# Performance work log

Hardware: AMD Instinct MI355X
Metric: run time of the kernel (lower is better)

Reference implementation:

```python
import math
import jax, jax.numpy as jnp
import numpy as np

MIN_AMT, MAX_AMT = 1, 32
C = 3
B, H, W = 128, 224, 224


def build_kernel_table():
    # kernels[i] has size = i + MIN_AMT: vertical center column, each channel sums to 1,
    # zero-padded (centered) to MAX_AMT x MAX_AMT (pad_to_width).
    tbl = np.zeros((MAX_AMT - MIN_AMT + 1, MAX_AMT, MAX_AMT, C), np.float32)
    for i, size in enumerate(range(MIN_AMT, MAX_AMT + 1)):
        pad = MAX_AMT - size
        t = pad // 2
        col = t + size // 2
        tbl[i, t:t + size, col, :] = 1.0 / size
    return jnp.asarray(tbl)


def setup_inputs() -> dict:
    key = jax.random.key(0)
    k1, k2, k3 = jax.random.split(key, 3)
    x = jax.random.uniform(k1, (B, H, W, C), jnp.float32)  # image batch
    amt = jax.random.randint(k2, (B,), MIN_AMT, MAX_AMT, dtype=jnp.int32)  # [min, max)
    angles = jax.random.randint(k3, (B,), 0, 91, dtype=jnp.int32)  # degrees [0, 91)
    return {"x": x, "kernels_table": build_kernel_table(), "amt": amt, "angles": angles}


def _rotate_nearest(img, rad):
    # img: (K, K, C); nearest-neighbor rotation about image center (tf.contrib.image.rotate
    # convention: output (x,y) samples input at [cos -sin; sin cos] @ (x,y) + centering offset).
    K = img.shape[0]
    cos, sin = jnp.cos(rad), jnp.sin(rad)
    coords = jnp.arange(K, dtype=jnp.float32)
    yy, xx = jnp.meshgrid(coords, coords, indexing="ij")
    e = jnp.float32(K - 1)
    x_off = (e - (cos * e - sin * e)) * 0.5
    y_off = (e - (sin * e + cos * e)) * 0.5
    sx = cos * xx - sin * yy + x_off
    sy = sin * xx + cos * yy + y_off
    ix = jnp.round(sx).astype(jnp.int32)
    iy = jnp.round(sy).astype(jnp.int32)
    valid = (ix >= 0) & (ix < K) & (iy >= 0) & (iy < K)
    g = img[jnp.clip(iy, 0, K - 1), jnp.clip(ix, 0, K - 1)]  # (K, K, C)
    return jnp.where(valid[..., None], g, jnp.float32(0.0))


def _depthwise_conv(img, ker):
    # img: (H, W, C); ker: (K, K, C) -> per-channel SAME conv, stride 1.
    out = jax.lax.conv_general_dilated(
        img[None], ker[:, :, None, :], (1, 1), "SAME",
        dimension_numbers=("NHWC", "HWIO", "NHWC"), feature_group_count=C)
    return out[0]


def reference(x, kernels_table, amt, angles):
    ker = kernels_table[amt]                                # (B, K, K, C) per-sample gather
    rad = angles.astype(jnp.float32) * jnp.float32(math.pi / 180.0)
    ker = jax.vmap(_rotate_nearest)(ker, rad)               # per-sample rotation
    out = jax.vmap(_depthwise_conv)(x, ker)                 # per-sample depthwise conv
    return out.reshape(-1, 224, 224, 3)
```

## Files before the change

### kernel.cpp

```cpp
#include <hip/hip_runtime.h>
#include <math.h>

namespace {

constexpr int Himg = 224, Wimg = 224, Cn = 3, Kk = 32;
constexpr int MAXT = 64;
constexpr int WSTRIDE = 512;
constexpr int IMG_F  = Himg * Wimg * Cn;
constexpr int ROW_F  = Wimg * Cn;
constexpr int ROW_B  = ROW_F * 4;

constexpr int TW_F = 224;
constexpr int TH = 32;
constexpr int RH = 16;
constexpr int TILES_X = 3;
constexpr int TILES_Y = 7;
constexpr int TPI = TILES_X * TILES_Y;
constexpr int L_W = 320;
constexpr int L_H = TH + 31;
constexpr int L_SZ = L_W * L_H;

typedef float v4  __attribute__((ext_vector_type(4), aligned(4)));
typedef float v4a __attribute__((ext_vector_type(4), aligned(16)));


__global__ __launch_bounds__(64)
void build_taps(const float* __restrict__ tbl,
                const int* __restrict__ amt,
                const int* __restrict__ ang,
                int* __restrict__ ws)
{
    const int b   = blockIdx.x;
    const int tid = threadIdx.x;

    __shared__ int   s_cnt;
    __shared__ float s_w;
    __shared__ int   s_dky[MAXT], s_dkx[MAXT];

    if (tid == 0) { s_cnt = 0; s_w = 0.0f; }
    __syncthreads();

    const int a = amt[b];
    const float  rad = (float)ang[b] * (float)(M_PI / 180.0);
    const double rd  = (double)rad;
    const float  cth = (float)cos(rd);
    const float  sth = (float)sin(rd);
    const float  e   = 31.0f;
    const float xoff = __fmul_rn(__fsub_rn(e, __fsub_rn(__fmul_rn(cth, e), __fmul_rn(sth, e))), 0.5f);
    const float yoff = __fmul_rn(__fsub_rn(e, __fadd_rn(__fmul_rn(sth, e), __fmul_rn(cth, e))), 0.5f);

    for (int p = tid; p < Kk * Kk; p += 64) {
        const int   ky = p >> 5, kx = p & 31;
        const float xf = (float)kx, yf = (float)ky;
        const float sx = __fadd_rn(__fsub_rn(__fmul_rn(cth, xf), __fmul_rn(sth, yf)), xoff);
        const float sy = __fadd_rn(__fadd_rn(__fmul_rn(sth, xf), __fmul_rn(cth, yf)), yoff);
        const int ix = (int)rintf(sx);
        const int iy = (int)rintf(sy);
        if (ix >= 0 && ix < Kk && iy >= 0 && iy < Kk) {
            const float v = tbl[((a * Kk + iy) * Kk + ix) * Cn];
            if (v != 0.0f) {
                const int idx = atomicAdd(&s_cnt, 1);
                if (idx < MAXT) {
                    s_dky[idx] = ky - 15;
                    s_dkx[idx] = kx - 15;
                    s_w = v;
                }
            }
        }
    }
    __syncthreads();

    const int n = min(s_cnt, MAXT);
    int* wsb = ws + b * WSTRIDE;
    if (tid == 0) { wsb[0] = n; wsb[1] = __float_as_int(s_w); }
    for (int i = tid; i < n; i += 64) {
        wsb[2 + i]   = s_dky[i];
        wsb[66 + i]  = s_dkx[i];
        wsb[130 + i] = s_dky[i] * ROW_B + s_dkx[i] * (int)(Cn * sizeof(float));
    }
}

__global__ __launch_bounds__(512, 2)
void blur_w8(const float* __restrict__ x,
             const int* __restrict__ ws,
             float* __restrict__ out,
             int B)
{
    const int tid = threadIdx.x;
    const int L   = blockIdx.x;

    int b, t;
    if (B == 128) {
        const int xcd = L & 7;
        const int j   = L >> 3;
        const int g   = j / TPI;
        t = j - g * TPI;
        b = g * 8 + xcd;
    } else {
        b = L / TPI;
        t = L - b * TPI;
    }
    const int ty = t / TILES_X;
    const int tx = t - ty * TILES_X;
    const int y0 = ty * TH;
    const int g0 = tx * TW_F - 48;
    const int r0 = y0 - 15;

    __shared__ float lds[L_SZ];
    __shared__ int   shNW[2];
    __shared__ int   s_tof[MAXT + 1];

    const int* wsb = ws + b * WSTRIDE;
    if (tid < 2)    shNW[tid] = wsb[tid];
    if (tid < MAXT) {
        const int dky = wsb[2 + tid];
        const int dkx = wsb[66 + tid];
        s_tof[tid] = (dky * L_W + 3 * dkx) * 4;
    }

    const float* xb = x + (size_t)b * IMG_F;
    for (int u = tid; u < L_H * 80; u += 512) {
        const int lr  = u / 80;
        const int lc4 = (u - lr * 80) * 4;
        const int gr  = r0 + lr;
        const int gc  = g0 + lc4;
        v4 val = {0.0f, 0.0f, 0.0f, 0.0f};
        if ((unsigned)gr < (unsigned)Himg && (unsigned)gc < (unsigned)ROW_F)
            val = *(const v4a*)(xb + (size_t)gr * ROW_F + gc);
        *(v4a*)(&lds[lr * L_W + lc4]) = val;
    }
    __syncthreads();

    const int   n = shNW[0];
    const float w = __int_as_float(shNW[1]);

    const int half = tid >> 8;
    const int col  = tid - (half << 8);

    if (col < TW_F) {
        const char* ldsb  = (const char*)lds;
        const int   abase = ((15 + half * RH) * L_W + 48 + col) * 4;

        float acc[RH];
#pragma unroll
        for (int p = 0; p < RH; ++p) acc[p] = 0.0f;

        int tofn = s_tof[0];
        for (int i = 0; i < n; ++i) {
            const int tof = __builtin_amdgcn_readfirstlane(tofn);
            tofn = s_tof[i + 1];
            const char* ap = ldsb + (abase + tof);
#pragma unroll
            for (int p = 0; p < RH; ++p) {
                acc[p] += *(const float*)(ap + p * (L_W * 4));
            }
        }

        float* ob = out + (size_t)b * IMG_F + (size_t)(y0 + half * RH) * ROW_F + tx * TW_F + col;
#pragma unroll
        for (int p = 0; p < RH; ++p) {
            __builtin_nontemporal_store(acc[p] * w, ob + p * ROW_F);
        }
    }
}

}

extern "C" void kernel_launch(void* const* d_in, const int* in_sizes, int n_in,
                              void* d_out, int out_size, void* d_ws, size_t ws_size,
                              hipStream_t stream) {
    const float* x   = (const float*)d_in[0];
    const float* tbl = (const float*)d_in[1];
    const int*   amt = (const int*)d_in[2];
    const int*   ang = (const int*)d_in[3];
    float*       out = (float*)d_out;
    int*         ws  = (int*)d_ws;

    const int B = in_sizes[2];

    build_taps<<<B, 64, 0, stream>>>(tbl, amt, ang, ws);
    blur_w8<<<B * TPI, 512, 0, stream>>>(x, ws, out, B);
}
```

Before: 185.7 us.

## Slide LDS window down column strips with register-prefetched rows

Each block now covers four 28-row tiles in a vertical strip instead of one 32-row tile. Between tiles it shifts the 31-row halo up in LDS and fills in newly loaded rows, and those rows are prefetched into registers while the current tile is being computed. This removes the repeated halo loads from global memory and overlaps loading with compute. In exchange the grid drops to 768 blocks, register pressure rises from the prefetch buffers, and two extra barriers are added per tile.

Result: no change. 189.3 us (+1.9%).

```diff
diff --git a/kernel.cpp b/kernel.cpp
--- a/kernel.cpp
+++ b/kernel.cpp
@@ -11,14 +11,17 @@
 constexpr int ROW_B  = ROW_F * 4;
 
 constexpr int TW_F = 224;
-constexpr int TH = 32;
-constexpr int RH = 16;
+constexpr int TH   = 28;
 constexpr int TILES_X = 3;
-constexpr int TILES_Y = 7;
-constexpr int TPI = TILES_X * TILES_Y;
-constexpr int L_W = 320;
-constexpr int L_H = TH + 31;
+constexpr int TPB  = 4;
+constexpr int RH   = TH / 2;
+constexpr int L_W  = 320;
+constexpr int L_H  = TH + 31;
 constexpr int L_SZ = L_W * L_H;
+constexpr int SH_ROWS = L_H - TH;
+constexpr int SH_CH   = SH_ROWS * 80;
+constexpr int NEW_CH  = TH * 80;
+constexpr int PRO_CH  = L_H * 80;
 
 typedef float v4  __attribute__((ext_vector_type(4), aligned(4)));
 typedef float v4a __attribute__((ext_vector_type(4), aligned(16)));
@@ -81,30 +84,29 @@
 }
 
 __global__ __launch_bounds__(512, 2)
-void blur_w8(const float* __restrict__ x,
-             const int* __restrict__ ws,
-             float* __restrict__ out,
-             int B)
+void blur_slide(const float* __restrict__ x,
+                const int* __restrict__ ws,
+                float* __restrict__ out,
+                int B)
 {
     const int tid = threadIdx.x;
     const int L   = blockIdx.x;
 
-    int b, t;
+    int b, rem;
     if (B == 128) {
         const int xcd = L & 7;
         const int j   = L >> 3;
-        const int g   = j / TPI;
-        t = j - g * TPI;
-        b = g * 8 + xcd;
+        const int g   = j / 6;
+        rem = j - g * 6;
+        b   = g * 8 + xcd;
     } else {
-        b = L / TPI;
-        t = L - b * TPI;
-    }
-    const int ty = t / TILES_X;
-    const int tx = t - ty * TILES_X;
-    const int y0 = ty * TH;
+        b   = L / 6;
+        rem = L - b * 6;
+    }
+    const int tx    = rem >> 1;
+    const int yhalf = rem & 1;
+    const int tyBeg = yhalf * TPB;
     const int g0 = tx * TW_F - 48;
-    const int r0 = y0 - 15;
 
     __shared__ float lds[L_SZ];
     __shared__ int   shNW[2];
@@ -119,48 +121,107 @@
     }
 
     const float* xb = x + (size_t)b * IMG_F;
-    for (int u = tid; u < L_H * 80; u += 512) {
-        const int lr  = u / 80;
-        const int lc4 = (u - lr * 80) * 4;
-        const int gr  = r0 + lr;
-        const int gc  = g0 + lc4;
-        v4 val = {0.0f, 0.0f, 0.0f, 0.0f};
-        if ((unsigned)gr < (unsigned)Himg && (unsigned)gc < (unsigned)ROW_F)
-            val = *(const v4a*)(xb + (size_t)gr * ROW_F + gc);
-        *(v4a*)(&lds[lr * L_W + lc4]) = val;
+
+    {
+        const int r0 = tyBeg * TH - 15;
+        for (int u = tid; u < PRO_CH; u += 512) {
+            const int lr  = u / 80;
+            const int lc4 = (u - lr * 80) * 4;
+            const int gr  = r0 + lr;
+            const int gc  = g0 + lc4;
+            const bool ok = (unsigned)gr < (unsigned)Himg && (unsigned)gc < (unsigned)ROW_F;
+            const float* sp = ok ? (xb + (size_t)gr * ROW_F + gc) : xb;
+            const v4 tv = *(const v4a*)sp;
+            *(v4a*)(&lds[4 * u]) = ok ? tv : v4{0, 0, 0, 0};
+        }
     }
     __syncthreads();
 
     const int   n = shNW[0];
     const float w = __int_as_float(shNW[1]);
-
-    const int half = tid >> 8;
-    const int col  = tid - (half << 8);
-
-    if (col < TW_F) {
-        const char* ldsb  = (const char*)lds;
-        const int   abase = ((15 + half * RH) * L_W + 48 + col) * 4;
-
-        float acc[RH];
-#pragma unroll
-        for (int p = 0; p < RH; ++p) acc[p] = 0.0f;
-
-        int tofn = s_tof[0];
-        for (int i = 0; i < n; ++i) {
-            const int tof = __builtin_amdgcn_readfirstlane(tofn);
-            tofn = s_tof[i + 1];
-            const char* ap = ldsb + (abase + tof);
-#pragma unroll
-            for (int p = 0; p < RH; ++p) {
-                acc[p] += *(const float*)(ap + p * (L_W * 4));
-            }
-        }
-
-        float* ob = out + (size_t)b * IMG_F + (size_t)(y0 + half * RH) * ROW_F + tx * TW_F + col;
-#pragma unroll
-        for (int p = 0; p < RH; ++p) {
-            __builtin_nontemporal_store(acc[p] * w, ob + p * ROW_F);
-        }
+    const int rhalf = tid >> 8;
+    const int col   = tid - (rhalf << 8);
+
+    for (int t = 0; t < TPB; ++t) {
+        const int y0 = (tyBeg + t) * TH;
+
+        v4 rv0{0,0,0,0}, rv1{0,0,0,0}, rv2{0,0,0,0}, rv3{0,0,0,0}, rv4{0,0,0,0};
+        if (t < TPB - 1) {
+#pragma unroll
+            for (int j = 0; j < 5; ++j) {
+                const int v = tid + 512 * j;
+                if (v < NEW_CH) {
+                    const int rr  = v / 80;
+                    const int cc4 = (v - rr * 80) * 4;
+                    const int gr  = y0 + TH + 16 + rr;
+                    const int gc  = g0 + cc4;
+                    const bool ok = (unsigned)gr < (unsigned)Himg && (unsigned)gc < (unsigned)ROW_F;
+                    const float* sp = ok ? (xb + (size_t)gr * ROW_F + gc) : xb;
+                    v4 tv = *(const v4a*)sp;
+                    tv = ok ? tv : v4{0, 0, 0, 0};
+                    if (j == 0) rv0 = tv; else if (j == 1) rv1 = tv; else if (j == 2) rv2 = tv;
+                    else if (j == 3) rv3 = tv; else rv4 = tv;
+                }
+            }
+        }
+
+        if (col < TW_F) {
+            const char* ldsb  = (const char*)lds;
+            const int   abase = ((15 + rhalf * RH) * L_W + 48 + col) * 4;
+
+            float acc[RH];
+#pragma unroll
+            for (int p = 0; p < RH; ++p) acc[p] = 0.0f;
+
+            int tofn = s_tof[0];
+            for (int i = 0; i < n; ++i) {
+                const int tof = __builtin_amdgcn_readfirstlane(tofn);
+                tofn = s_tof[i + 1];
+                const char* ap = ldsb + (abase + tof);
+#pragma unroll
+                for (int p = 0; p < RH; ++p)
+                    acc[p] += *(const float*)(ap + p * (L_W * 4));
+            }
+
+            float* ob = out + (size_t)b * IMG_F
+                      + (size_t)(y0 + rhalf * RH) * ROW_F + tx * TW_F + col;
+#pragma unroll
+            for (int p = 0; p < RH; ++p)
+                __builtin_nontemporal_store(acc[p] * w, ob + p * ROW_F);
+        }
+        if (t == TPB - 1) break;
+
+        v4 sv0{0,0,0,0}, sv1{0,0,0,0}, sv2{0,0,0,0}, sv3{0,0,0,0}, sv4{0,0,0,0};
+#pragma unroll
+        for (int j = 0; j < 5; ++j) {
+            const int v = tid + 512 * j;
+            if (v < SH_CH) {
+                const v4 tv = *(const v4a*)(&lds[TH * L_W + 4 * v]);
+                if (j == 0) sv0 = tv; else if (j == 1) sv1 = tv; else if (j == 2) sv2 = tv;
+                else if (j == 3) sv3 = tv; else sv4 = tv;
+            }
+        }
+        __syncthreads();
+
+#pragma unroll
+        for (int j = 0; j < 5; ++j) {
+            const int v = tid + 512 * j;
+            if (v < SH_CH) {
+                const v4 tv = (j == 0) ? sv0 : (j == 1) ? sv1 : (j == 2) ? sv2
+                            : (j == 3) ? sv3 : sv4;
+                *(v4a*)(&lds[4 * v]) = tv;
+            }
+        }
+#pragma unroll
+        for (int j = 0; j < 5; ++j) {
+            const int v = tid + 512 * j;
+            if (v < NEW_CH) {
+                const v4 tv = (j == 0) ? rv0 : (j == 1) ? rv1 : (j == 2) ? rv2
+                            : (j == 3) ? rv3 : rv4;
+                *(v4a*)(&lds[SH_ROWS * L_W + 4 * v]) = tv;
+            }
+        }
+        __syncthreads();
     }
 }
 
@@ -179,5 +240,5 @@
     const int B = in_sizes[2];
 
     build_taps<<<B, 64, 0, stream>>>(tbl, amt, ang, ws);
-    blur_w8<<<B * TPI, 512, 0, stream>>>(x, ws, out, B);
-}
+    blur_slide<<<B * TILES_X * 2, 512, 0, stream>>>(x, ws, out, B);
+}
```
